# Kernel optimization log

Measured on AMD Instinct MI355X. Metric: run time of the kernel, lower is better.

The kernel has to match this reference:

```python
import jax, jax.numpy as jnp
import numpy as np

DIM = 2048
KV_DIM = 1024
NUM_HEADS = 16
HEAD_DIM = DIM // NUM_HEADS  # 128
EPS = 1e-6
B, LQ, LKV = 2, 4096, 1024


def _rope_cos_sin(L, d, base=10000.0):
    inv_freq = 1.0 / (base ** (np.arange(0, d, 2, dtype=np.float32) / d))  # [d/2]
    freqs = np.arange(L, dtype=np.float32)[:, None] * inv_freq[None, :]   # [L, d/2]
    emb = np.concatenate([freqs, freqs], axis=-1)                          # [L, d]
    return jnp.asarray(np.cos(emb)), jnp.asarray(np.sin(emb))


def setup_inputs() -> dict:
    key = jax.random.key(0)
    ks = jax.random.split(key, 10)
    x = jax.random.normal(ks[0], (B, LQ, DIM), dtype=jnp.float32)
    y = jax.random.normal(ks[1], (B, LKV, KV_DIM), dtype=jnp.float32)
    xc, xs = _rope_cos_sin(LQ, HEAD_DIM)
    yc, ys = _rope_cos_sin(LKV, HEAD_DIM)
    x_cos = jnp.broadcast_to(xc[None], (B, LQ, HEAD_DIM))
    x_sin = jnp.broadcast_to(xs[None], (B, LQ, HEAD_DIM))
    y_cos = jnp.broadcast_to(yc[None], (B, LKV, HEAD_DIM))
    y_sin = jnp.broadcast_to(ys[None], (B, LKV, HEAD_DIM))
    s = 0.02
    Wq = jax.random.normal(ks[2], (DIM, DIM), dtype=jnp.float32) * s
    Wk = jax.random.normal(ks[3], (DIM, KV_DIM), dtype=jnp.float32) * s
    Wv = jax.random.normal(ks[4], (DIM, KV_DIM), dtype=jnp.float32) * s
    Wo = jax.random.normal(ks[5], (DIM, DIM), dtype=jnp.float32) * s
    bq = jnp.zeros((DIM,), jnp.float32)
    bk = jnp.zeros((DIM,), jnp.float32)
    bv = jnp.zeros((DIM,), jnp.float32)
    bo = jnp.zeros((DIM,), jnp.float32)
    rmsq_w = jnp.ones((DIM,), jnp.float32)
    rmsk_w = jnp.ones((DIM,), jnp.float32)
    ln_w = jnp.ones((KV_DIM,), jnp.float32)
    ln_b = jnp.zeros((KV_DIM,), jnp.float32)
    return dict(x=x, y=y, x_cos=x_cos, x_sin=x_sin, y_cos=y_cos, y_sin=y_sin,
                Wq=Wq, bq=bq, Wk=Wk, bk=bk, Wv=Wv, bv=bv, Wo=Wo, bo=bo,
                rmsq_w=rmsq_w, rmsk_w=rmsk_w, ln_w=ln_w, ln_b=ln_b)


def _rms_norm(t, w, eps=EPS):
    return t * jax.lax.rsqrt(jnp.mean(t * t, axis=-1, keepdims=True) + eps) * w


def _layer_norm(t, w, b, eps=EPS):
    mu = jnp.mean(t, axis=-1, keepdims=True)
    var = jnp.mean(jnp.square(t - mu), axis=-1, keepdims=True)
    return (t - mu) * jax.lax.rsqrt(var + eps) * w + b


def _rotate_half(t):
    d2 = t.shape[-1] // 2
    return jnp.concatenate([-t[..., d2:], t[..., :d2]], axis=-1)


def _apply_rope(t, cos, sin):
    # t: [B, L, H, D]; cos/sin: [B, L, D] -> unsqueeze head dim (unsqueeze_dim=2)
    cos = cos[:, :, None, :]
    sin = sin[:, :, None, :]
    return t * cos + _rotate_half(t) * sin


def _block_forward(x, y, x_cos, x_sin, y_cos, y_sin,
                   Wq, bq, Wk, bk, Wv, bv, Wo, bo,
                   rmsq_w, rmsk_w, ln_w, ln_b):
    Bb, Lq, D = x.shape
    Lk = y.shape[1]
    H, Dh = NUM_HEADS, HEAD_DIM
    # y pre-norm (block-level LayerNorm)
    yn = _layer_norm(y, ln_w, ln_b)
    # projections + RMSNorm on q/k
    q = _rms_norm(x @ Wq.T + bq, rmsq_w)   # [B, Lq, D]
    k = _rms_norm(yn @ Wk.T + bk, rmsk_w)  # [B, Lk, D]
    v = yn @ Wv.T + bv                     # [B, Lk, D]
    # split heads and apply RoPE
    q = _apply_rope(q.reshape(Bb, Lq, H, Dh), x_cos, x_sin)
    k = _apply_rope(k.reshape(Bb, Lk, H, Dh), y_cos, y_sin)
    v = v.reshape(Bb, Lk, H, Dh)
    # non-causal cross attention, scale = 1/sqrt(head_dim)
    scale = 1.0 / jnp.sqrt(jnp.asarray(Dh, q.dtype))
    scores = jnp.einsum('blhd,bmhd->bhlm', q, k) * scale
    probs = jax.nn.softmax(scores, axis=-1)
    out = jnp.einsum('bhlm,bmhd->blhd', probs, v).reshape(Bb, Lq, D)
    return out @ Wo.T + bo


def reference(x, y, x_cos, x_sin, y_cos, y_sin,
              Wq, bq, Wk, bk, Wv, bv, Wo, bo,
              rmsq_w, rmsk_w, ln_w, ln_b):
    return _block_forward(x, y, x_cos, x_sin, y_cos, y_sin,
                          Wq, bq, Wk, bk, Wv, bv, Wo, bo,
                          rmsq_w, rmsk_w, ln_w, ln_b)
```

## Files before the change

### kernel.cpp

```cpp
#include <hip/hip_runtime.h>


typedef __attribute__((ext_vector_type(8))) short    short8;
typedef __attribute__((ext_vector_type(8))) unsigned short ushort8;
typedef __attribute__((ext_vector_type(4))) unsigned short ushort4v;
typedef __attribute__((ext_vector_type(4))) float    f32x4;
typedef __attribute__((ext_vector_type(16))) float   f32x16;
typedef __attribute__((ext_vector_type(4))) unsigned int uint4v;

#define DEV __device__ __forceinline__

DEV unsigned short f2bf(float f) {
  unsigned int u = __builtin_bit_cast(unsigned int, f);
  u += 0x7FFFu + ((u >> 16) & 1u);
  return (unsigned short)(u >> 16);
}
DEV float bf2f(unsigned short h) {
  return __builtin_bit_cast(float, ((unsigned int)h) << 16);
}
DEV unsigned int cvtpk_bf16(float lo, float hi) {
  unsigned int r;
  asm("v_cvt_pk_bf16_f32 %0, %1, %2" : "=v"(r) : "v"(lo), "v"(hi));
  return r;
}
DEV short8 mk8(unsigned a, unsigned b, unsigned c, unsigned d) {
  uint4v t; t.x = a; t.y = b; t.z = c; t.w = d;
  return __builtin_bit_cast(short8, t);
}

DEV void gload_lds16(const void* g, void* l) {
  __builtin_amdgcn_global_load_lds(
      (const __attribute__((address_space(1))) void*)g,
      (__attribute__((address_space(3))) void*)l, 16, 0, 0);
}

__global__ __launch_bounds__(256) void cvt_kernel(const float* __restrict__ in,
                                                  unsigned short* __restrict__ out,
                                                  int n4) {
  int idx = blockIdx.x * 256 + threadIdx.x;
  int stride = gridDim.x * 256;
  for (int i = idx; i < n4; i += stride) {
    float4 v = *(const float4*)(in + (size_t)i * 4);
    ushort4v o;
    o.x = f2bf(v.x); o.y = f2bf(v.y); o.z = f2bf(v.z); o.w = f2bf(v.w);
    *(ushort4v*)(out + (size_t)i * 4) = o;
  }
}

__global__ __launch_bounds__(256) void ln_kernel(const float* __restrict__ y,
                                                 const float* __restrict__ w,
                                                 const float* __restrict__ b,
                                                 unsigned short* __restrict__ yn) {
  const int row = blockIdx.x;
  const int t = threadIdx.x;
  const float* yr = y + (size_t)row * 1024;
  float4 v = *(const float4*)(yr + t * 4);
  float s1 = v.x + v.y + v.z + v.w;
  float s2 = v.x * v.x + v.y * v.y + v.z * v.z + v.w * v.w;
#pragma unroll
  for (int m = 1; m < 64; m <<= 1) {
    s1 += __shfl_xor(s1, m);
    s2 += __shfl_xor(s2, m);
  }
  __shared__ float red[8];
  const int wave = t >> 6, lane = t & 63;
  if (lane == 0) { red[wave] = s1; red[4 + wave] = s2; }
  __syncthreads();
  s1 = red[0] + red[1] + red[2] + red[3];
  s2 = red[4] + red[5] + red[6] + red[7];
  const float mu = s1 * (1.0f / 1024.0f);
  const float var = s2 * (1.0f / 1024.0f) - mu * mu;
  const float rs = rsqrtf(var + 1e-6f);
  ushort4v o;
  o.x = f2bf((v.x - mu) * rs * w[t * 4 + 0] + b[t * 4 + 0]);
  o.y = f2bf((v.y - mu) * rs * w[t * 4 + 1] + b[t * 4 + 1]);
  o.z = f2bf((v.z - mu) * rs * w[t * 4 + 2] + b[t * 4 + 2]);
  o.w = f2bf((v.w - mu) * rs * w[t * 4 + 3] + b[t * 4 + 3]);
  *(ushort4v*)(yn + (size_t)row * 1024 + t * 4) = o;
}

__global__ __launch_bounds__(256) void gemm_bt(const unsigned short* __restrict__ A,
                                               const unsigned short* __restrict__ W,
                                               const float* __restrict__ bias0,
                                               const float* __restrict__ bias1,
                                               int nsplit,
                                               unsigned short* __restrict__ Cout,
                                               int M, int N, int K) {
  __shared__ __align__(16) char sA[128 * 128];
  __shared__ __align__(16) char sB[128 * 128];
  const int tid = threadIdx.x;
  const int wave = tid >> 6, lane = tid & 63;
  const int lg = lane >> 4, l15 = lane & 15;
  const int wr = wave >> 1, wc = wave & 1;
  const int m0 = blockIdx.y * 128;
  const int n0 = blockIdx.x * 128;
  const char* Ab = (const char*)A;
  const char* Wb = (const char*)W;
  const size_t ldab = (size_t)K * 2;

  f32x4 acc[4][4] = {};

  for (int kt = 0; kt < K; kt += 64) {
#pragma unroll
    for (int i = 0; i < 4; ++i) {
      const int p = (i * 256 + tid) * 16;
      const int row = p >> 7;
      const int si = (p & 127) ^ ((row & 7) << 4);
      gload_lds16(Ab + (size_t)(m0 + row) * ldab + (size_t)kt * 2 + si, sA + p);
    }
#pragma unroll
    for (int i = 0; i < 4; ++i) {
      const int p = (i * 256 + tid) * 16;
      const int row = p >> 7;
      const int si = (p & 127) ^ ((row & 7) << 4);
      gload_lds16(Wb + (size_t)(n0 + row) * ldab + (size_t)kt * 2 + si, sB + p);
    }
    __syncthreads();
#pragma unroll
    for (int ks = 0; ks < 2; ++ks) {
      const int kb = (ks * 32 + lg * 8) * 2;
      short8 af[4], bw[4];
#pragma unroll
      for (int mf = 0; mf < 4; ++mf) {
        const int row = wr * 64 + mf * 16 + l15;
        af[mf] = *(const short8*)(sA + row * 128 + (kb ^ ((row & 7) << 4)));
      }
#pragma unroll
      for (int nf = 0; nf < 4; ++nf) {
        const int row = wc * 64 + nf * 16 + l15;
        bw[nf] = *(const short8*)(sB + row * 128 + (kb ^ ((row & 7) << 4)));
      }
#pragma unroll
      for (int mf = 0; mf < 4; ++mf)
#pragma unroll
        for (int nf = 0; nf < 4; ++nf)
          acc[mf][nf] = __builtin_amdgcn_mfma_f32_16x16x32_bf16(af[mf], bw[nf],
                                                                acc[mf][nf], 0, 0, 0);
    }
    __syncthreads();
  }

#pragma unroll
  for (int nf = 0; nf < 4; ++nf) {
    const int n = n0 + wc * 64 + nf * 16 + l15;
    const float bv = (n < nsplit) ? bias0[n] : bias1[n - nsplit];
#pragma unroll
    for (int mf = 0; mf < 4; ++mf) {
      const int mB = m0 + wr * 64 + mf * 16 + lg * 4;
#pragma unroll
      for (int r = 0; r < 4; ++r)
        Cout[(size_t)(mB + r) * N + n] = f2bf(acc[mf][nf][r] + bv);
    }
  }
}

template <int EPI>
__global__ __launch_bounds__(512, 2) void gemm256(const unsigned short* __restrict__ A,
                                                  const unsigned short* __restrict__ W,
                                                  const float* __restrict__ bias,
                                                  void* __restrict__ Cout,
                                                  int M, int N, int K) {
  __shared__ __align__(16) char lds[2][4][16384];
  const int tid = threadIdx.x;
  const int wave = tid >> 6, lane = tid & 63;
  const int lg = lane >> 4, l15 = lane & 15;
  const int wm = wave >> 2, wn = wave & 3;

  const int nwg = gridDim.x;
  const int wgid = (blockIdx.x & 7) * (nwg >> 3) + (blockIdx.x >> 3);
  const int nbn = N >> 8;
  const int m0 = (wgid / nbn) * 256;
  const int n0 = (wgid % nbn) * 256;

  const char* Ab = (const char*)A;
  const char* Wb = (const char*)W;
  const size_t ld = (size_t)K * 2;
  const int NT = K >> 6;
  const int NI = NT >> 1;

  const int prow = tid >> 3;
  const int psw  = ((tid * 16) & 127) ^ ((prow & 7) << 4);
  const int pdst = tid * 16;
  const char* pAg = Ab + (size_t)(m0 + prow) * ld + psw;
  const char* pBg = Wb + (size_t)(n0 + prow) * ld + psw;

  f32x4 acc[8][4] = {};
  short8 af[4][2];
  short8 bf[4][2];

#define STG(BUF, HALF, ISB, TAU) do {                                         \
    const char* _g = ((ISB) ? pBg : pAg) + (size_t)(HALF) * 128 * ld +        \
                     (size_t)(TAU) * 128;                                     \
    char* _l = lds[BUF][(ISB) * 2 + (HALF)];                                  \
    gload_lds16(_g, _l + pdst);                                               \
    gload_lds16(_g + 64 * ld, _l + pdst + 8192);                              \
  } while (0)

#define LDA(BUF, H) do {                                                      \
    const char* _b = lds[BUF][wm];                                            \
    _Pragma("unroll") for (int mfl = 0; mfl < 4; ++mfl) {                     \
      const int _r = (H) * 64 + mfl * 16 + l15;                               \
      _Pragma("unroll") for (int ks = 0; ks < 2; ++ks)                        \
        af[mfl][ks] = *(const short8*)(_b + _r * 128 +                        \
                        ((ks * 64 + lg * 16) ^ ((_r & 7) << 4)));             \
    }                                                                         \
  } while (0)

#define LDB(BUF, G) do {                                                      \
    const char* _b = lds[BUF][2 + (wn >> 1)];                                 \
    _Pragma("unroll") for (int nfl = 0; nfl < 2; ++nfl) {                     \
      const int _r = (wn & 1) * 64 + (G) * 32 + nfl * 16 + l15;               \
      _Pragma("unroll") for (int ks = 0; ks < 2; ++ks)                        \
        bf[(G) * 2 + nfl][ks] = *(const short8*)(_b + _r * 128 +              \
                        ((ks * 64 + lg * 16) ^ ((_r & 7) << 4)));             \
    }                                                                         \
  } while (0)

#define MFMA_Q(H, G) do {                                                     \
    __builtin_amdgcn_s_setprio(1);                                            \
    _Pragma("unroll") for (int ks = 0; ks < 2; ++ks)                          \
    _Pragma("unroll") for (int mfl = 0; mfl < 4; ++mfl)                       \
    _Pragma("unroll") for (int nfl = 0; nfl < 2; ++nfl)                       \
      acc[(H) * 4 + mfl][(G) * 2 + nfl] =                                     \
        __builtin_amdgcn_mfma_f32_16x16x32_bf16(af[mfl][ks],                  \
            bf[(G) * 2 + nfl][ks], acc[(H) * 4 + mfl][(G) * 2 + nfl], 0,0,0); \
    __builtin_amdgcn_s_setprio(0);                                            \
  } while (0)

#define BAR() __builtin_amdgcn_s_barrier()
#define LGKM0() do { asm volatile("s_waitcnt lgkmcnt(0)" ::: "memory");       \
    __builtin_amdgcn_sched_barrier(0); } while (0)
#define VM4() asm volatile("s_waitcnt vmcnt(4)" ::: "memory")
#define VM0() asm volatile("s_waitcnt vmcnt(0)" ::: "memory")

  STG(0, 0, 0, 0); STG(0, 1, 0, 0); STG(0, 0, 1, 0); STG(0, 1, 1, 0);
  STG(1, 0, 1, 1); STG(1, 1, 1, 1);
  VM4(); BAR();

  for (int t = 0; t < NI - 1; ++t) {
    const int t2 = 2 * t;
    LDA(0, 0); LDB(0, 0); STG(1, 0, 0, t2 + 1);
    BAR(); LGKM0(); MFMA_Q(0, 0); BAR();
    LDB(0, 1); STG(1, 1, 0, t2 + 1);
    BAR(); LGKM0(); MFMA_Q(0, 1); BAR();
    LDA(0, 1); STG(0, 0, 1, t2 + 2);
    BAR(); LGKM0(); MFMA_Q(1, 1); BAR();
    STG(0, 1, 1, t2 + 2);
    BAR(); MFMA_Q(1, 0); VM4(); BAR();
    LDA(1, 0); LDB(1, 0); STG(0, 0, 0, t2 + 2);
    BAR(); LGKM0(); MFMA_Q(0, 0); BAR();
    LDB(1, 1); STG(0, 1, 0, t2 + 2);
    BAR(); LGKM0(); MFMA_Q(0, 1); BAR();
    LDA(1, 1); STG(1, 0, 1, t2 + 3);
    BAR(); LGKM0(); MFMA_Q(1, 1); BAR();
    STG(1, 1, 1, t2 + 3);
    BAR(); MFMA_Q(1, 0); VM4(); BAR();
  }

  LDA(0, 0); LDB(0, 0); STG(1, 0, 0, NT - 1);
  BAR(); LGKM0(); MFMA_Q(0, 0); BAR();
  LDB(0, 1); STG(1, 1, 0, NT - 1);
  BAR(); LGKM0(); MFMA_Q(0, 1); BAR();
  LDA(0, 1);
  BAR(); LGKM0(); MFMA_Q(1, 1); BAR();
  BAR(); MFMA_Q(1, 0); VM0(); BAR();
  LDA(1, 0); LDB(1, 0); LGKM0(); MFMA_Q(0, 0);
  LDB(1, 1); LGKM0(); MFMA_Q(0, 1);
  LDA(1, 1); LGKM0(); MFMA_Q(1, 1);
  MFMA_Q(1, 0);

#undef STG
#undef LDA
#undef LDB
#undef MFMA_Q
#undef BAR
#undef LGKM0
#undef VM4
#undef VM0

#pragma unroll
  for (int nf = 0; nf < 4; ++nf) {
    const int n = n0 + wn * 64 + nf * 16 + l15;
    const float bv = bias[n];
#pragma unroll
    for (int mf = 0; mf < 8; ++mf) {
      const int mB = m0 + wm * 128 + mf * 16 + lg * 4;
#pragma unroll
      for (int r = 0; r < 4; ++r) {
        const float v = acc[mf][nf][r] + bv;
        if constexpr (EPI == 0)
          ((unsigned short*)Cout)[(size_t)(mB + r) * N + n] = f2bf(v);
        else
          ((float*)Cout)[(size_t)(mB + r) * N + n] = v;
      }
    }
  }
}

__global__ __launch_bounds__(256) void rmsrope_kernel(const unsigned short* __restrict__ in,
                                                      const float* __restrict__ w,
                                                      const float* __restrict__ cs,
                                                      const float* __restrict__ sn,
                                                      unsigned short* __restrict__ out,
                                                      int L, int ldin, float scale) {
  const int row = blockIdx.x;
  const int t = threadIdx.x;
  __shared__ __align__(16) unsigned short srow[2048];
  __shared__ float red[4];
  const unsigned short* ir = in + (size_t)row * ldin;
  ushort8 v = *(const ushort8*)(ir + t * 8);
  float vals[8];
  float ss = 0.f;
#pragma unroll
  for (int j = 0; j < 8; ++j) { vals[j] = bf2f(v[j]); ss += vals[j] * vals[j]; }
  *(ushort8*)(srow + t * 8) = v;
#pragma unroll
  for (int m = 1; m < 64; m <<= 1) ss += __shfl_xor(ss, m);
  const int wave = t >> 6, lane = t & 63;
  if (lane == 0) red[wave] = ss;
  __syncthreads();
  const float tot = red[0] + red[1] + red[2] + red[3];
  const float rms = rsqrtf(tot * (1.0f / 2048.0f) + 1e-6f);

  const int n0 = t * 8;
  const int d0 = n0 & 127;
  const int hh = n0 >> 7;
  const float sign = (d0 < 64) ? -1.0f : 1.0f;
  const float* cb = cs + (size_t)row * 128 + d0;
  const float* sb = sn + (size_t)row * 128 + d0;
  ushort8 po = *(const ushort8*)(srow + (n0 ^ 64));
  ushort8 ou;
#pragma unroll
  for (int j = 0; j < 8; ++j) {
    const float self = vals[j] * rms * w[n0 + j];
    const float part = bf2f(po[j]) * rms * w[(n0 ^ 64) + j];
    ou[j] = f2bf((self * cb[j] + sign * part * sb[j]) * scale);
  }
  const int b = row / L, l = row - (row / L) * L;
  *(ushort8*)(out + (((size_t)(b * 16 + hh)) * L + l) * 128 + d0) = ou;
}

__global__ __launch_bounds__(256) void vtrans_kernel(const unsigned short* __restrict__ vpre,
                                                     unsigned short* __restrict__ vt,
                                                     int ldv) {
  const int bid = blockIdx.x;
  const int kt = bid & 15, bh = bid >> 4;
  const int h = bh & 15, b = bh >> 4;
  __shared__ unsigned short lt[64][130];
  const int t = threadIdx.x;
  const int i0 = t >> 4, c0 = (t & 15) * 8;
  const unsigned short* src = vpre + ((size_t)(b * 1024 + kt * 64)) * ldv + h * 128;
#pragma unroll
  for (int ii = 0; ii < 4; ++ii) {
    const int i = i0 + ii * 16;
    ushort8 v = *(const ushort8*)(src + (size_t)i * ldv + c0);
#pragma unroll
    for (int j = 0; j < 8; ++j) lt[i][c0 + j] = v[j];
  }
  __syncthreads();
  const int d0 = t >> 3, j0 = (t & 7) * 8;
  unsigned short* dst = vt + (size_t)bh * 128 * 1024 + kt * 64;
#pragma unroll
  for (int dd = 0; dd < 4; ++dd) {
    const int d = d0 + dd * 32;
    ushort8 o;
#pragma unroll
    for (int jj = 0; jj < 8; ++jj) o[jj] = lt[j0 + jj][d];
    *(ushort8*)(dst + (size_t)d * 1024 + j0) = o;
  }
}

__global__ __launch_bounds__(512, 2) void attn_kernel(const unsigned short* __restrict__ q,
                                                      const unsigned short* __restrict__ k,
                                                      const unsigned short* __restrict__ vt,
                                                      unsigned short* __restrict__ ao) {
  __shared__ __align__(16) char sK[2][64 * 256];
  __shared__ __align__(16) char sV[2][128 * 128];

  const int bid0 = blockIdx.x;
  const int bid = (bid0 & 7) * 64 + (bid0 >> 3);
  const int qt = bid & 15, bh = bid >> 4;
  const int tid = threadIdx.x;
  const int wave = tid >> 6, lane = tid & 63;
  const int l31 = lane & 31, hi = lane >> 5;
  const bool hib = (hi != 0);

  const unsigned short* qbase = q + (((size_t)bh * 4096) + qt * 256 + wave * 32) * 128;
  const char* kbase = (const char*)(k + (size_t)bh * 1024 * 128);
  const char* vbase = (const char*)(vt + (size_t)bh * 128 * 1024);

  short8 qb[8];
#pragma unroll
  for (int step = 0; step < 8; ++step)
    qb[step] = *(const short8*)(qbase + (size_t)l31 * 128 + step * 16 + hi * 8);

  f32x16 o[4] = {};
  float lsum = 0.f;

#define STAGE_KV(BUF, KV0) do {                                              \
    _Pragma("unroll")                                                        \
    for (int i = 0; i < 2; ++i) {                                            \
      const int p = (i * 512 + tid) * 16;                                    \
      const int row = p >> 8;                                                \
      const int si = (p & 255) ^ ((row & 7) << 4);                           \
      gload_lds16(kbase + (size_t)((KV0) + row) * 256 + si, sK[BUF] + p);    \
    }                                                                        \
    _Pragma("unroll")                                                        \
    for (int i = 0; i < 2; ++i) {                                            \
      const int p = (i * 512 + tid) * 16;                                    \
      const int row = p >> 7;                                                \
      const int si = (p & 127) ^ ((row & 7) << 4);                           \
      gload_lds16(vbase + (size_t)row * 2048 + (KV0) * 2 + si, sV[BUF] + p); \
    }                                                                        \
  } while (0)

#define SOFTMAX_PV(SS, F) do {                                               \
    float p_[16];                                                            \
    _Pragma("unroll") for (int r = 0; r < 16; ++r) p_[r] = exp2f((SS)[r]);   \
    lsum += ((p_[0]+p_[1])+(p_[2]+p_[3])) + ((p_[4]+p_[5])+(p_[6]+p_[7]))    \
          + ((p_[8]+p_[9])+(p_[10]+p_[11])) + ((p_[12]+p_[13])+(p_[14]+p_[15]));\
    const unsigned w0 = cvtpk_bf16(p_[0], p_[1]),  w1 = cvtpk_bf16(p_[2], p_[3]), \
                   w2 = cvtpk_bf16(p_[4], p_[5]),  w3 = cvtpk_bf16(p_[6], p_[7]), \
                   w4 = cvtpk_bf16(p_[8], p_[9]),  w5 = cvtpk_bf16(p_[10], p_[11]),\
                   w6 = cvtpk_bf16(p_[12], p_[13]),w7 = cvtpk_bf16(p_[14], p_[15]);\
    const unsigned x0 = (unsigned)__shfl_xor((int)(hib ? w0 : w2), 32);      \
    const unsigned x1 = (unsigned)__shfl_xor((int)(hib ? w1 : w3), 32);      \
    const unsigned x2 = (unsigned)__shfl_xor((int)(hib ? w4 : w6), 32);      \
    const unsigned x3 = (unsigned)__shfl_xor((int)(hib ? w5 : w7), 32);      \
    const short8 fr0 = mk8(hib ? x0 : w0, hib ? x1 : w1,                     \
                           hib ? w2 : x0, hib ? w3 : x1);                    \
    const short8 fr1 = mk8(hib ? x2 : w4, hib ? x3 : w5,                     \
                           hib ? w6 : x2, hib ? w7 : x3);                    \
    __builtin_amdgcn_s_setprio(1);                                           \
    _Pragma("unroll") for (int kstep = 0; kstep < 2; ++kstep) {              \
      const short8 pa = kstep ? fr1 : fr0;                                   \
      const int col = (F) * 64 + kstep * 32 + hi * 16;                       \
      _Pragma("unroll") for (int dt = 0; dt < 4; ++dt) {                     \
        const int vrow = dt * 32 + l31;                                      \
        short8 vf = *(const short8*)(V + vrow * 128 +                        \
                                     (col ^ ((vrow & 7) << 4)));             \
        o[dt] = __builtin_amdgcn_mfma_f32_32x32x16_bf16(pa, vf, o[dt], 0,0,0);\
      }                                                                      \
    }                                                                        \
    __builtin_amdgcn_s_setprio(0);                                           \
  } while (0)

  STAGE_KV(0, 0);
  __syncthreads();

  int cur = 0;
  for (int kt = 0; kt < 16; ++kt) {
    if (kt < 15) STAGE_KV(cur ^ 1, (kt + 1) * 64);

    const char* const K = sK[cur];
    const char* const V = sV[cur];

    f32x16 s0 = {}, s1 = {};
    const int krow0 = l31, krow1 = 32 + l31;
    const int ksw0 = (krow0 & 7) << 4, ksw1 = (krow1 & 7) << 4;
    __builtin_amdgcn_s_setprio(1);
#pragma unroll
    for (int step = 0; step < 8; ++step) {
      const int cb2 = step * 32 + hi * 16;
      short8 kf0 = *(const short8*)(K + krow0 * 256 + (cb2 ^ ksw0));
      short8 kf1 = *(const short8*)(K + krow1 * 256 + (cb2 ^ ksw1));
      s0 = __builtin_amdgcn_mfma_f32_32x32x16_bf16(kf0, qb[step], s0, 0, 0, 0);
      s1 = __builtin_amdgcn_mfma_f32_32x32x16_bf16(kf1, qb[step], s1, 0, 0, 0);
    }
    __builtin_amdgcn_s_setprio(0);

    SOFTMAX_PV(s0, 0);
    SOFTMAX_PV(s1, 1);

    __syncthreads();
    cur ^= 1;
  }
#undef STAGE_KV
#undef SOFTMAX_PV

  lsum += __shfl_xor(lsum, 32);
  const float linv = 1.0f / lsum;
  const int b = bh >> 4, h = bh & 15;
#pragma unroll
  for (int r = 0; r < 16; ++r) {
    const int crow = (r & 3) + 8 * (r >> 2) + 4 * hi;
    const float inv = __shfl(linv, crow);
    const int qg = qt * 256 + wave * 32 + crow;
    const size_t orow = ((size_t)b * 4096 + qg) * 2048 + h * 128;
#pragma unroll
    for (int dt = 0; dt < 4; ++dt)
      ao[orow + dt * 32 + l31] = f2bf(o[dt][r] * inv);
  }
}

extern "C" void kernel_launch(void* const* d_in, const int* in_sizes, int n_in,
                              void* d_out, int out_size, void* d_ws, size_t ws_size,
                              hipStream_t stream) {
  (void)in_sizes; (void)n_in; (void)out_size; (void)ws_size;
  const float* x      = (const float*)d_in[0];
  const float* y      = (const float*)d_in[1];
  const float* x_cos  = (const float*)d_in[2];
  const float* x_sin  = (const float*)d_in[3];
  const float* y_cos  = (const float*)d_in[4];
  const float* y_sin  = (const float*)d_in[5];
  const float* Wq     = (const float*)d_in[6];
  const float* bq     = (const float*)d_in[7];
  const float* Wk     = (const float*)d_in[8];
  const float* bk     = (const float*)d_in[9];
  const float* Wv     = (const float*)d_in[10];
  const float* bv     = (const float*)d_in[11];
  const float* Wo     = (const float*)d_in[12];
  const float* bo     = (const float*)d_in[13];
  const float* rmsq_w = (const float*)d_in[14];
  const float* rmsk_w = (const float*)d_in[15];
  const float* ln_w   = (const float*)d_in[16];
  const float* ln_b   = (const float*)d_in[17];

  char* ws = (char*)d_ws;
  unsigned short* xb    = (unsigned short*)(ws + 0);
  unsigned short* Wqb   = (unsigned short*)(ws + 33554432);
  unsigned short* Wkb   = (unsigned short*)(ws + 41943040);
  unsigned short* Wvb   = (unsigned short*)(ws + 46137344);
  unsigned short* Wob   = (unsigned short*)(ws + 50331648);
  unsigned short* ynb   = (unsigned short*)(ws + 58720256);
  unsigned short* kvpre = (unsigned short*)(ws + 62914560);
  unsigned short* qpre  = (unsigned short*)(ws + 62914560);
  unsigned short* qr    = (unsigned short*)(ws + 96468992);
  unsigned short* kr    = (unsigned short*)(ws + 130023424);
  unsigned short* vt    = (unsigned short*)(ws + 138412032);
  unsigned short* ao    = xb;

  const float qscale = 1.4426950408889634f * 0.08838834764831843f;

  cvt_kernel<<<2048, 256, 0, stream>>>(x, xb, (2 * 4096 * 2048) / 4);
  cvt_kernel<<<512, 256, 0, stream>>>(Wq, Wqb, (2048 * 2048) / 4);
  cvt_kernel<<<512, 256, 0, stream>>>(Wk, Wkb, (2048 * 1024) / 4);
  cvt_kernel<<<512, 256, 0, stream>>>(Wv, Wvb, (2048 * 1024) / 4);
  cvt_kernel<<<512, 256, 0, stream>>>(Wo, Wob, (2048 * 2048) / 4);
  ln_kernel<<<2048, 256, 0, stream>>>(y, ln_w, ln_b, ynb);

  dim3 gKV(32, 16);
  gemm_bt<<<gKV, 256, 0, stream>>>(ynb, Wkb, bk, bv, 2048, kvpre, 2048, 4096, 1024);
  rmsrope_kernel<<<2048, 256, 0, stream>>>(kvpre, rmsk_w, y_cos, y_sin, kr, 1024, 4096, 1.0f);
  vtrans_kernel<<<512, 256, 0, stream>>>(kvpre + 2048, vt, 4096);

  gemm256<0><<<256, 512, 0, stream>>>(xb, Wqb, bq, qpre, 8192, 2048, 2048);
  rmsrope_kernel<<<8192, 256, 0, stream>>>(qpre, rmsq_w, x_cos, x_sin, qr, 4096, 2048, qscale);

  attn_kernel<<<512, 512, 0, stream>>>(qr, kr, vt, ao);

  gemm256<1><<<256, 512, 0, stream>>>(ao, Wob, bo, (float*)d_out, 8192, 2048, 2048);
}
```

Measured before the change: 325.8 us.

## Compute softmax row sums via MFMA with ones and reshape V LDS layout

```diff
diff --git a/kernel.cpp b/kernel.cpp
--- a/kernel.cpp
+++ b/kernel.cpp
@@ -370,12 +370,12 @@
   }
 }
 
-__global__ __launch_bounds__(512, 2) void attn_kernel(const unsigned short* __restrict__ q,
+__global__ __launch_bounds__(512, 4) void attn_kernel(const unsigned short* __restrict__ q,
                                                       const unsigned short* __restrict__ k,
                                                       const unsigned short* __restrict__ vt,
                                                       unsigned short* __restrict__ ao) {
   __shared__ __align__(16) char sK[2][64 * 256];
-  __shared__ __align__(16) char sV[2][128 * 128];
+  __shared__ __align__(16) char sV[2][64 * 256];
 
   const int bid0 = blockIdx.x;
   const int bid = (bid0 & 7) * 64 + (bid0 >> 3);
@@ -395,30 +395,31 @@
     qb[step] = *(const short8*)(qbase + (size_t)l31 * 128 + step * 16 + hi * 8);
 
   f32x16 o[4] = {};
-  float lsum = 0.f;
+  f32x16 ol = {};
+  const short8 vones = mk8(0x3F803F80u, 0x3F803F80u, 0x3F803F80u, 0x3F803F80u);
 
 #define STAGE_KV(BUF, KV0) do {                                              \
     _Pragma("unroll")                                                        \
     for (int i = 0; i < 2; ++i) {                                            \
       const int p = (i * 512 + tid) * 16;                                    \
       const int row = p >> 8;                                                \
-      const int si = (p & 255) ^ ((row & 7) << 4);                           \
+      const int si = (p & 255) ^ ((row & 15) << 4);                          \
       gload_lds16(kbase + (size_t)((KV0) + row) * 256 + si, sK[BUF] + p);    \
     }                                                                        \
     _Pragma("unroll")                                                        \
     for (int i = 0; i < 2; ++i) {                                            \
       const int p = (i * 512 + tid) * 16;                                    \
-      const int row = p >> 7;                                                \
-      const int si = (p & 127) ^ ((row & 7) << 4);                           \
-      gload_lds16(vbase + (size_t)row * 2048 + (KV0) * 2 + si, sV[BUF] + p); \
+      const int row = p >> 8;                                                \
+      const int si = (p & 255) ^ ((row & 15) << 4);                          \
+      const int d = 2 * row + (si >> 7);                                     \
+      gload_lds16(vbase + (size_t)d * 2048 + (KV0) * 2 + (si & 127),         \
+                  sV[BUF] + p);                                              \
     }                                                                        \
   } while (0)
 
-#define SOFTMAX_PV(SS, F) do {                                               \
+#define SOFTMAX_PV(V, SS, F) do {                                            \
     float p_[16];                                                            \
     _Pragma("unroll") for (int r = 0; r < 16; ++r) p_[r] = exp2f((SS)[r]);   \
-    lsum += ((p_[0]+p_[1])+(p_[2]+p_[3])) + ((p_[4]+p_[5])+(p_[6]+p_[7]))    \
-          + ((p_[8]+p_[9])+(p_[10]+p_[11])) + ((p_[12]+p_[13])+(p_[14]+p_[15]));\
     const unsigned w0 = cvtpk_bf16(p_[0], p_[1]),  w1 = cvtpk_bf16(p_[2], p_[3]), \
                    w2 = cvtpk_bf16(p_[4], p_[5]),  w3 = cvtpk_bf16(p_[6], p_[7]), \
                    w4 = cvtpk_bf16(p_[8], p_[9]),  w5 = cvtpk_bf16(p_[10], p_[11]),\
@@ -434,57 +435,58 @@
     __builtin_amdgcn_s_setprio(1);                                           \
     _Pragma("unroll") for (int kstep = 0; kstep < 2; ++kstep) {              \
       const short8 pa = kstep ? fr1 : fr0;                                   \
-      const int col = (F) * 64 + kstep * 32 + hi * 16;                       \
+      const int colb = (F) * 64 + kstep * 32 + hi * 16;                      \
       _Pragma("unroll") for (int dt = 0; dt < 4; ++dt) {                     \
-        const int vrow = dt * 32 + l31;                                      \
-        short8 vf = *(const short8*)(V + vrow * 128 +                        \
-                                     (col ^ ((vrow & 7) << 4)));             \
+        const int vrow = dt * 16 + (l31 >> 1);                               \
+        const int inner = (l31 & 1) * 128 + colb;                            \
+        short8 vf = *(const short8*)((V) + vrow * 256 +                      \
+                                     (inner ^ ((vrow & 15) << 4)));          \
         o[dt] = __builtin_amdgcn_mfma_f32_32x32x16_bf16(pa, vf, o[dt], 0,0,0);\
       }                                                                      \
+      ol = __builtin_amdgcn_mfma_f32_32x32x16_bf16(pa, vones, ol, 0, 0, 0);  \
     }                                                                        \
     __builtin_amdgcn_s_setprio(0);                                           \
   } while (0)
 
+#define TILE(BUF) do {                                                       \
+    const char* const K = sK[BUF];                                           \
+    const char* const V = sV[BUF];                                           \
+    f32x16 s0 = {}, s1 = {};                                                 \
+    const int ksw = (l31 & 15) << 4;                                         \
+    __builtin_amdgcn_s_setprio(1);                                           \
+    _Pragma("unroll") for (int step = 0; step < 8; ++step) {                 \
+      const int cb2 = step * 32 + hi * 16;                                   \
+      short8 kf0 = *(const short8*)(K + l31 * 256 + (cb2 ^ ksw));            \
+      short8 kf1 = *(const short8*)(K + (32 + l31) * 256 + (cb2 ^ ksw));     \
+      s0 = __builtin_amdgcn_mfma_f32_32x32x16_bf16(kf0, qb[step], s0, 0,0,0);\
+      s1 = __builtin_amdgcn_mfma_f32_32x32x16_bf16(kf1, qb[step], s1, 0,0,0);\
+    }                                                                        \
+    __builtin_amdgcn_s_setprio(0);                                           \
+    SOFTMAX_PV(V, s0, 0);                                                    \
+    SOFTMAX_PV(V, s1, 1);                                                    \
+  } while (0)
+
   STAGE_KV(0, 0);
   __syncthreads();
 
-  int cur = 0;
-  for (int kt = 0; kt < 16; ++kt) {
-    if (kt < 15) STAGE_KV(cur ^ 1, (kt + 1) * 64);
-
-    const char* const K = sK[cur];
-    const char* const V = sV[cur];
-
-    f32x16 s0 = {}, s1 = {};
-    const int krow0 = l31, krow1 = 32 + l31;
-    const int ksw0 = (krow0 & 7) << 4, ksw1 = (krow1 & 7) << 4;
-    __builtin_amdgcn_s_setprio(1);
-#pragma unroll
-    for (int step = 0; step < 8; ++step) {
-      const int cb2 = step * 32 + hi * 16;
-      short8 kf0 = *(const short8*)(K + krow0 * 256 + (cb2 ^ ksw0));
-      short8 kf1 = *(const short8*)(K + krow1 * 256 + (cb2 ^ ksw1));
-      s0 = __builtin_amdgcn_mfma_f32_32x32x16_bf16(kf0, qb[step], s0, 0, 0, 0);
-      s1 = __builtin_amdgcn_mfma_f32_32x32x16_bf16(kf1, qb[step], s1, 0, 0, 0);
-    }
-    __builtin_amdgcn_s_setprio(0);
-
-    SOFTMAX_PV(s0, 0);
-    SOFTMAX_PV(s1, 1);
-
+#pragma unroll 1
+  for (int kt2 = 0; kt2 < 8; ++kt2) {
+    STAGE_KV(1, (2 * kt2 + 1) * 64);
+    TILE(0);
     __syncthreads();
-    cur ^= 1;
+    if (kt2 < 7) STAGE_KV(0, (2 * kt2 + 2) * 64);
+    TILE(1);
+    __syncthreads();
   }
 #undef STAGE_KV
 #undef SOFTMAX_PV
-
-  lsum += __shfl_xor(lsum, 32);
-  const float linv = 1.0f / lsum;
+#undef TILE
+
   const int b = bh >> 4, h = bh & 15;
 #pragma unroll
   for (int r = 0; r < 16; ++r) {
     const int crow = (r & 3) + 8 * (r >> 2) + 4 * hi;
-    const float inv = __shfl(linv, crow);
+    const float inv = 1.0f / ol[r];
     const int qg = qt * 256 + wave * 32 + crow;
     const size_t orow = ((size_t)b * 4096 + qg) * 2048 + h * 128;
 #pragma unroll
```

New measurement: 798.5 us. 2.45x slower.
